# Performance work log

Measured on AMD Instinct MI355X. Metric: run time of the kernel, lower is better.

## Reference

```python
import jax, jax.numpy as jnp
import numpy as np

B, V, J, NB = 512, 6890, 24, 10
P = (J - 1) * 9  # 207 pose-blendshape features
# Standard SMPL kinematic tree (parents[0] = -1 for root)
PARENTS = np.array([-1, 0, 0, 0, 1, 2, 3, 4, 5, 6, 7, 8, 9, 9, 9, 12, 13, 14, 16, 17, 18, 19, 20, 21])


def rodrigues(aa):
    """Axis-angle [N,3] -> rotation matrices [N,3,3] (batch_rodrigues)."""
    angle = jnp.linalg.norm(aa, axis=-1, keepdims=True) + 1e-8
    axis = aa / angle
    x, y, z = axis[..., 0], axis[..., 1], axis[..., 2]
    zero = jnp.zeros_like(x)
    K = jnp.stack([zero, -z, y, z, zero, -x, -y, x, zero], axis=-1).reshape(aa.shape[0], 3, 3)
    s = jnp.sin(angle)[..., None]
    c = jnp.cos(angle)[..., None]
    return jnp.eye(3, dtype=aa.dtype) + s * K + (1.0 - c) * jnp.matmul(K, K)


def setup_inputs() -> dict:
    key = jax.random.key(0)
    ks = jax.random.split(key, 9)
    J_reg = jax.random.uniform(ks[7], (J, V), dtype=jnp.float32)
    J_reg = J_reg / jnp.sum(J_reg, axis=1, keepdims=True)
    W = jax.nn.softmax(4.0 * jax.random.normal(ks[8], (V, J), dtype=jnp.float32), axis=-1)
    return {
        "betas": jax.random.normal(ks[0], (B, NB), dtype=jnp.float32),
        "body_pose": 0.3 * jax.random.normal(ks[1], (B, (J - 1) * 3), dtype=jnp.float32),
        "global_orient": 0.3 * jax.random.normal(ks[2], (B, 3), dtype=jnp.float32),
        "transl": jax.random.normal(ks[3], (B, 3), dtype=jnp.float32),
        "v_template": jax.random.normal(ks[4], (V, 3), dtype=jnp.float32),
        "shapedirs": 0.01 * jax.random.normal(ks[5], (V, 3, NB), dtype=jnp.float32),
        "posedirs": 0.01 * jax.random.normal(ks[6], (P, V * 3), dtype=jnp.float32),
        "J_regressor": J_reg,
        "lbs_weights": W,
    }


def reference(betas, body_pose, global_orient, transl, v_template, shapedirs, posedirs, J_regressor, lbs_weights):
    b = betas.shape[0]
    # --- pose to rotation matrices (pose2rot=True path) ---
    full_pose = jnp.concatenate([global_orient, body_pose], axis=-1)  # [B, 72]
    rot_mats = rodrigues(full_pose.reshape(-1, 3)).reshape(b, J, 3, 3)
    # --- shape blend shapes ---
    v_shaped = v_template + jnp.einsum('bl,vcl->bvc', betas, shapedirs)  # [B,V,3]
    joints = jnp.einsum('jv,bvc->bjc', J_regressor, v_shaped)            # [B,J,3]
    # --- pose blend shapes ---
    pose_feature = (rot_mats[:, 1:] - jnp.eye(3, dtype=rot_mats.dtype)).reshape(b, P)
    v_posed = v_shaped + (pose_feature @ posedirs).reshape(b, V, 3)
    # --- kinematic chain (batch_rigid_transform) ---
    rel_joints = joints.at[:, 1:].add(-joints[:, PARENTS[1:]])
    top = jnp.concatenate([rot_mats, rel_joints[..., None]], axis=-1)   # [B,J,3,4]
    bottom = jnp.broadcast_to(jnp.array([0.0, 0.0, 0.0, 1.0], dtype=rot_mats.dtype), (b, J, 1, 4))
    mats = jnp.concatenate([top, bottom], axis=-2)                      # [B,J,4,4]
    chain = [mats[:, 0]]
    for i in range(1, J):  # fixed 24-joint serial composition
        chain.append(chain[PARENTS[i]] @ mats[:, i])
    A = jnp.stack(chain, axis=1)                                        # [B,J,4,4]
    posed_joints = A[..., :3, 3]
    # remove rest-pose joint locations from the transforms
    t_rel = A[..., :3, 3] - jnp.einsum('bjmn,bjn->bjm', A[..., :3, :3], joints)
    A_rel = A.at[..., :3, 3].set(t_rel)
    # --- linear blend skinning ---
    T = jnp.einsum('vj,bjmn->bvmn', lbs_weights, A_rel)                 # [B,V,4,4]
    verts = jnp.einsum('bvmn,bvn->bvm', T[..., :3, :3], v_posed) + T[..., :3, 3]
    vertices = verts + transl[:, None]
    joints_out = posed_joints + transl[:, None]
    return vertices, joints_out
```

## Files before the change

### kernel.cpp

```cpp
#include <hip/hip_runtime.h>
#include <hip/hip_bf16.h>
#include <math.h>

#define Bn 512
#define Vn 6890
#define NBn 10
#define Pn 207
#define N3n 20670
#define KP 224
#define VPAD 6912

typedef __attribute__((ext_vector_type(8))) _Float16 half8;
typedef __attribute__((ext_vector_type(4))) float f32x4;

__constant__ int c_par[24] = {-1,0,0,0,1,2,3,4,5,6,7,8,9,9,9,12,13,14,16,17,18,19,20,21};
__constant__ int c_lvl[10] = {0,1,4,7,10,15,18,20,22,24};


__global__ __launch_bounds__(256) void k_prep(
    const float* __restrict__ Jreg, const float* __restrict__ vtpl,
    const float* __restrict__ sdirs, const float* __restrict__ pdirs,
    const float* __restrict__ W, float* __restrict__ part,
    _Float16* __restrict__ B_h, _Float16* __restrict__ W_h)
{
  const int tid = threadIdx.x;
  if (blockIdx.x < 576) {
    const int bid = blockIdx.x % 72;
    const int chunk = blockIdx.x / 72;
    const int j = bid / 3, c = bid % 3;
    const int vlo = chunk * 862;
    const int vhi = min(Vn, vlo + 862);
    float acc[11];
#pragma unroll
    for (int k = 0; k < 11; k++) acc[k] = 0.f;
    for (int v = vlo + tid; v < vhi; v += 256) {
      float w = Jreg[(size_t)j * Vn + v];
      int n = v * 3 + c;
#pragma unroll
      for (int l = 0; l < 10; l++) acc[l] += w * sdirs[(size_t)n * 10 + l];
      acc[10] += w * vtpl[n];
    }
    __shared__ float red[256];
    for (int k = 0; k < 11; k++) {
      red[tid] = acc[k];
      __syncthreads();
      for (int s = 128; s > 0; s >>= 1) {
        if (tid < s) red[tid] += red[tid + s];
        __syncthreads();
      }
      if (tid == 0) part[(size_t)chunk * 792 + bid * 11 + k] = red[0];
      __syncthreads();
    }
  } else if (blockIdx.x < 576 + 2268) {
    const int pair = (blockIdx.x - 576) * 4 + (tid >> 6);
    const int l = tid & 63;
    const int nt = pair / 7, s = pair % 7;
    const int col = nt * 16 + (l & 15);
    const int kb = s * 32 + ((l >> 4) << 3);
    half8 hv;
#pragma unroll
    for (int j = 0; j < 8; j++) {
      int k = kb + j;
      float f = 0.f;
      if (col < N3n) {
        if (k < Pn) f = pdirs[(size_t)k * N3n + col];
        else if (k < 217) f = sdirs[(size_t)col * 10 + (k - 207)];
        else if (k == 217) f = (float)(_Float16)vtpl[col];
        else if (k == 218) {
          float t = vtpl[col];
          f = t - (float)(_Float16)t;
        }
      }
      hv[j] = (_Float16)f;
    }
    *(half8*)(B_h + (size_t)pair * 512 + l * 8) = hv;
  } else {
    int idx = (blockIdx.x - 576 - 2268) * 256 + tid;
    if (idx < VPAD * 32) {
      int v = idx >> 5, k = idx & 31;
      float f = (v < Vn && k < 24) ? W[(size_t)v * 24 + k] : 0.f;
      W_h[idx] = (_Float16)f;
    }
  }
}

__global__ __launch_bounds__(512) void k_pose2(
    const float* __restrict__ betas, const float* __restrict__ body_pose,
    const float* __restrict__ gorient, const float* __restrict__ transl,
    const float* __restrict__ part,
    _Float16* __restrict__ pf_h, _Float16* __restrict__ Ar_h,
    float* __restrict__ out_joints)
{
  const int tid = threadIdx.x;
  const int wave = tid >> 6;
  const int lane = tid & 63;
  const int b = blockIdx.x * 8 + wave;

  __shared__ float JS_s[720];
  __shared__ float Jt_s[72];
  __shared__ float Rs[8][24][9];
  __shared__ float jnt[8][24][3];
  __shared__ float rel[8][24][3];
  __shared__ float A_s[8][24][12];

  for (int idx = tid; idx < 792; idx += 512) {
    float s = 0.f;
#pragma unroll
    for (int y = 0; y < 8; y++) s += part[(size_t)y * 792 + idx];
    int bid = idx / 11, k = idx % 11;
    if (k < 10) JS_s[bid * 10 + k] = s;
    else        Jt_s[bid] = s;
  }

  if (lane < 24) {
    float x, y, z;
    if (lane == 0) { x = gorient[b*3+0]; y = gorient[b*3+1]; z = gorient[b*3+2]; }
    else { int o = b*69 + (lane-1)*3; x = body_pose[o]; y = body_pose[o+1]; z = body_pose[o+2]; }
    float ang = sqrtf(x*x + y*y + z*z) + 1e-8f;
    float inv = 1.0f / ang;
    float ux = x*inv, uy = y*inv, uz = z*inv;
    float s = sinf(ang), cc = cosf(ang), omc = 1.0f - cc;
    float K[9] = {0.f, -uz, uy,  uz, 0.f, -ux,  -uy, ux, 0.f};
#pragma unroll
    for (int mm = 0; mm < 3; mm++)
#pragma unroll
      for (int nn = 0; nn < 3; nn++) {
        float kk = K[mm*3+0]*K[0+nn] + K[mm*3+1]*K[3+nn] + K[mm*3+2]*K[6+nn];
        float eye = (mm == nn) ? 1.0f : 0.0f;
        Rs[wave][lane][mm*3+nn] = eye + s*K[mm*3+nn] + omc*kk;
      }
  }
  __syncthreads();

  for (int idx = lane; idx < 72; idx += 64) {
    float a = Jt_s[idx];
#pragma unroll
    for (int l = 0; l < 10; l++) a += betas[b*10 + l] * JS_s[idx*10 + l];
    jnt[wave][idx/3][idx%3] = a;
  }
  for (int idx = lane; idx < KP; idx += 64) {
    float f = 0.f;
    if (idx < Pn) {
      int j = 1 + idx / 9, e = idx % 9;
      float eye = (e == 0 || e == 4 || e == 8) ? 1.0f : 0.0f;
      f = Rs[wave][j][e] - eye;
    } else if (idx < 217) {
      f = betas[b*10 + (idx - 207)];
    } else if (idx < 219) {
      f = 1.0f;
    }
    pf_h[(size_t)b * KP + idx] = (_Float16)f;
  }
  __syncthreads();
  for (int idx = lane; idx < 72; idx += 64) {
    int j = idx/3, cc = idx%3;
    float r = jnt[wave][j][cc];
    if (j > 0) r -= jnt[wave][c_par[j]][cc];
    rel[wave][j][cc] = r;
  }
  __syncthreads();
  if (lane < 12) {
    int m = lane/4, nn = lane%4;
    A_s[wave][0][lane] = (nn < 3) ? Rs[wave][0][m*3+nn] : rel[wave][0][m];
  }
  __syncthreads();
  for (int lev = 1; lev <= 8; lev++) {
    const int s0 = c_lvl[lev], s1 = c_lvl[lev + 1];
    const int jj = lane / 12, r = lane % 12;
    if (jj < s1 - s0) {
      const int i = s0 + jj;
      const int p = c_par[i];
      const int m = r >> 2, nn = r & 3;
      float v;
      if (nn < 3)
        v = A_s[wave][p][m*4+0]*Rs[wave][i][0+nn] + A_s[wave][p][m*4+1]*Rs[wave][i][3+nn] + A_s[wave][p][m*4+2]*Rs[wave][i][6+nn];
      else
        v = A_s[wave][p][m*4+0]*rel[wave][i][0] + A_s[wave][p][m*4+1]*rel[wave][i][1] + A_s[wave][p][m*4+2]*rel[wave][i][2] + A_s[wave][p][m*4+3];
      A_s[wave][i][r] = v;
    }
    __syncthreads();
  }
  for (int idx = lane; idx < 72; idx += 64) {
    int j = idx/3, cc = idx%3;
    out_joints[(size_t)b * 72 + idx] = A_s[wave][j][cc*4+3] + transl[b*3+cc];
  }
  for (int idx = lane; idx < 512; idx += 64) {
    int e = idx >> 5, k = idx & 31;
    float a = 0.f;
    if (e < 12 && k < 24) {
      int m = e >> 2, nn = e & 3;
      if (nn < 3) a = A_s[wave][k][m*4+nn];
      else a = A_s[wave][k][m*4+3] - (A_s[wave][k][m*4+0]*jnt[wave][k][0] + A_s[wave][k][m*4+1]*jnt[wave][k][1] + A_s[wave][k][m*4+2]*jnt[wave][k][2]);
    }
    Ar_h[(size_t)b * 512 + idx] = (_Float16)a;
  }
}

__global__ __launch_bounds__(256) void k_mm3(
    const float* __restrict__ transl,
    const _Float16* __restrict__ pf_h, const _Float16* __restrict__ B_h,
    const _Float16* __restrict__ W_h, const _Float16* __restrict__ Ar_h,
    float* __restrict__ out)
{
  const int lin = blockIdx.x;
  const int r8 = lin & 7;
  const int k2 = lin >> 3;
  const int b_t = k2 & 7;
  const int m8 = k2 >> 3;
  const int v_t = r8 * 14 + m8;
  if (v_t >= 108) return;

  const int tid = threadIdx.x;
  const int l = tid & 63;
  const int wave = tid >> 6;
  const int b0 = b_t * 64;
  const int v0 = v_t * 64;

  __shared__ __align__(16) float vp[64][196];
  __shared__ float transl_s[64][3];

  if (tid < 192) transl_s[tid / 3][tid % 3] = transl[(size_t)b0 * 3 + tid];

  const int c0 = l & 15;
  const int kk0 = (l >> 4) << 3;
  const int ntb = v_t * 12 + wave * 3;
  f32x4 acc[4][3];
#pragma unroll
  for (int t = 0; t < 4; t++)
#pragma unroll
    for (int n = 0; n < 3; n++) acc[t][n] = (f32x4){0.f, 0.f, 0.f, 0.f};

#pragma unroll
  for (int s = 0; s < 7; s++) {
    half8 bv[3];
#pragma unroll
    for (int n = 0; n < 3; n++)
      bv[n] = *(const half8*)(B_h + ((size_t)(ntb + n) * 7 + s) * 512 + l * 8);
#pragma unroll
    for (int t = 0; t < 4; t++) {
      half8 fa = *(const half8*)(pf_h + (size_t)(b0 + t * 16 + c0) * KP + kk0 + s * 32);
#pragma unroll
      for (int n = 0; n < 3; n++)
        acc[t][n] = __builtin_amdgcn_mfma_f32_16x16x32_f16(fa, bv[n], acc[t][n], 0, 0, 0);
    }
  }
  {
    const int colb = wave * 48 + c0;
    const int rowb = (l >> 4) * 4;
#pragma unroll
    for (int t = 0; t < 4; t++)
#pragma unroll
      for (int n = 0; n < 3; n++)
#pragma unroll
        for (int r = 0; r < 4; r++)
          vp[t * 16 + rowb + r][colb + n * 16] = acc[t][n][r];
  }
  __syncthreads();

  const int c = l & 15;
  const int g = l >> 4;
  const int kk = g << 3;

  half8 wh[4];
#pragma unroll
  for (int mt = 0; mt < 4; mt++)
    wh[mt] = *(const half8*)(W_h + (size_t)(v0 + mt * 16 + c) * 32 + kk);

#pragma unroll
  for (int i = 0; i < 16; i++) {
    const int bl = wave * 16 + i;
    half8 ah = *(const half8*)(Ar_h + (size_t)(b0 + bl) * 512 + c * 32 + kk);
    const float trg = transl_s[bl][g < 3 ? g : 0];
#pragma unroll
    for (int mt = 0; mt < 4; mt++) {
      f32x4 t = {0.f, 0.f, 0.f, 0.f};
      t = __builtin_amdgcn_mfma_f32_16x16x32_f16(ah, wh[mt], t, 0, 0, 0);
      const int vl2 = mt * 16 + c;
      const int v = v0 + vl2;
      if (g < 3 && v < Vn) {
        float x = vp[bl][3 * vl2 + 0];
        float y = vp[bl][3 * vl2 + 1];
        float z = vp[bl][3 * vl2 + 2];
        out[((size_t)(b0 + bl) * Vn + v) * 3 + g] = t[0]*x + t[1]*y + t[2]*z + t[3] + trg;
      }
    }
  }
}


__global__ __launch_bounds__(256) void k_jsjt_part(
    const float* __restrict__ Jreg, const float* __restrict__ vtpl,
    const float* __restrict__ sdirs, float* __restrict__ part)
{
  const int bid = blockIdx.x;
  const int chunk = blockIdx.y;
  const int j = bid / 3, c = bid % 3;
  const int tid = threadIdx.x;
  const int vlo = chunk * 862;
  const int vhi = min(Vn, vlo + 862);
  float acc[11];
#pragma unroll
  for (int k = 0; k < 11; k++) acc[k] = 0.f;
  for (int v = vlo + tid; v < vhi; v += 256) {
    float w = Jreg[(size_t)j * Vn + v];
    int n = v * 3 + c;
#pragma unroll
    for (int l = 0; l < 10; l++) acc[l] += w * sdirs[(size_t)n * 10 + l];
    acc[10] += w * vtpl[n];
  }
  __shared__ float red[256];
  for (int k = 0; k < 11; k++) {
    red[tid] = acc[k];
    __syncthreads();
    for (int s = 128; s > 0; s >>= 1) {
      if (tid < s) red[tid] += red[tid + s];
      __syncthreads();
    }
    if (tid == 0) part[(size_t)chunk * 792 + bid * 11 + k] = red[0];
    __syncthreads();
  }
}

__global__ __launch_bounds__(1024) void k_jsjt_red(
    const float* __restrict__ part, float* __restrict__ JS, float* __restrict__ Jt)
{
  const int t = threadIdx.x;
  if (t >= 792) return;
  float s = 0.f;
#pragma unroll
  for (int y = 0; y < 8; y++) s += part[(size_t)y * 792 + t];
  int bid = t / 11, k = t % 11;
  if (k < 10) JS[bid * 10 + k] = s;
  else        Jt[bid] = s;
}

__global__ __launch_bounds__(64) void k_pose_fb(
    const float* __restrict__ betas, const float* __restrict__ body_pose,
    const float* __restrict__ gorient, const float* __restrict__ transl,
    const float* __restrict__ JS, const float* __restrict__ Jt,
    float* __restrict__ pf_ws, float* __restrict__ Ar_ws,
    float* __restrict__ out_joints)
{
  const int b = blockIdx.x;
  const int tid = threadIdx.x;
  __shared__ float Rs[24][9];
  __shared__ float jnt[24][3];
  __shared__ float rel[24][3];
  __shared__ float A_s[24][12];

  if (tid < 24) {
    float x, y, z;
    if (tid == 0) { x = gorient[b*3+0]; y = gorient[b*3+1]; z = gorient[b*3+2]; }
    else { int o = b*69 + (tid-1)*3; x = body_pose[o]; y = body_pose[o+1]; z = body_pose[o+2]; }
    float ang = sqrtf(x*x + y*y + z*z) + 1e-8f;
    float inv = 1.0f / ang;
    float ux = x*inv, uy = y*inv, uz = z*inv;
    float s = sinf(ang), cc = cosf(ang), omc = 1.0f - cc;
    float K[9] = {0.f, -uz, uy,  uz, 0.f, -ux,  -uy, ux, 0.f};
#pragma unroll
    for (int mm = 0; mm < 3; mm++)
#pragma unroll
      for (int nn = 0; nn < 3; nn++) {
        float kk = K[mm*3+0]*K[0+nn] + K[mm*3+1]*K[3+nn] + K[mm*3+2]*K[6+nn];
        float eye = (mm == nn) ? 1.0f : 0.0f;
        Rs[tid][mm*3+nn] = eye + s*K[mm*3+nn] + omc*kk;
      }
  }
  for (int idx = tid; idx < 72; idx += 64) {
    float a = Jt[idx];
#pragma unroll
    for (int l = 0; l < 10; l++) a += betas[b*10 + l] * JS[idx*10 + l];
    jnt[idx/3][idx%3] = a;
  }
  __syncthreads();
  for (int idx = tid; idx < Pn; idx += 64) {
    int j = 1 + idx / 9, e = idx % 9;
    float eye = (e == 0 || e == 4 || e == 8) ? 1.0f : 0.0f;
    pf_ws[(size_t)b * Pn + idx] = Rs[j][e] - eye;
  }
  for (int idx = tid; idx < 72; idx += 64) {
    int j = idx/3, cc = idx%3;
    float r = jnt[j][cc];
    if (j > 0) r -= jnt[c_par[j]][cc];
    rel[j][cc] = r;
  }
  __syncthreads();
  if (tid < 12) {
    int m = tid/4, nn = tid%4;
    A_s[0][tid] = (nn < 3) ? Rs[0][m*3+nn] : rel[0][m];
  }
  __syncthreads();
  for (int i = 1; i < 24; i++) {
    if (tid < 12) {
      int m = tid/4, nn = tid%4;
      int p = c_par[i];
      float v;
      if (nn < 3)
        v = A_s[p][m*4+0]*Rs[i][0+nn] + A_s[p][m*4+1]*Rs[i][3+nn] + A_s[p][m*4+2]*Rs[i][6+nn];
      else
        v = A_s[p][m*4+0]*rel[i][0] + A_s[p][m*4+1]*rel[i][1] + A_s[p][m*4+2]*rel[i][2] + A_s[p][m*4+3];
      A_s[i][tid] = v;
    }
    __syncthreads();
  }
  for (int idx = tid; idx < 72; idx += 64) {
    int j = idx/3, cc = idx%3;
    out_joints[(size_t)b * 72 + idx] = A_s[j][cc*4+3] + transl[b*3+cc];
  }
  for (int idx = tid; idx < 288; idx += 64) {
    int j = idx/12, r = idx%12, m = r/4, nn = r%4;
    float v;
    if (nn < 3) v = A_s[j][m*4+nn];
    else v = A_s[j][m*4+3] - (A_s[j][m*4+0]*jnt[j][0] + A_s[j][m*4+1]*jnt[j][1] + A_s[j][m*4+2]*jnt[j][2]);
    Ar_ws[(size_t)b * 288 + idx] = v;
  }
}

__global__ __launch_bounds__(192) void k_verts_fb(
    const float* __restrict__ betas, const float* __restrict__ transl,
    const float* __restrict__ vtpl, const float* __restrict__ sdirs,
    const float* __restrict__ pdirs, const float* __restrict__ W,
    const float* __restrict__ pf_ws, const float* __restrict__ Ar_ws,
    float* __restrict__ out)
{
  const int tid = threadIdx.x;
  const int b0 = blockIdx.x * 16;
  const int v0 = blockIdx.y * 128;
  const int n0 = v0 * 3;
  __shared__ __align__(16) float pf_s[Pn][16];
  __shared__ __align__(16) float Ar_s[16][288];
  __shared__ __align__(16) float vp_s[16][384];
  __shared__ float betas_s[16][NBn];
  __shared__ float transl_s[16][3];
  for (int idx = tid; idx < Pn * 16; idx += 192) {
    int p = idx >> 4, bi = idx & 15;
    pf_s[p][bi] = pf_ws[(size_t)(b0 + bi) * Pn + p];
  }
  for (int idx = tid; idx < 16 * 288; idx += 192)
    Ar_s[idx / 288][idx % 288] = Ar_ws[(size_t)b0 * 288 + idx];
  for (int idx = tid; idx < 16 * NBn; idx += 192)
    betas_s[idx / NBn][idx % NBn] = betas[(size_t)b0 * NBn + idx];
  for (int idx = tid; idx < 48; idx += 192)
    transl_s[idx / 3][idx % 3] = transl[(size_t)b0 * 3 + idx];
  __syncthreads();
  const int n = n0 + 2 * tid;
  const bool valid = (n < N3n);
  float acc0[16], acc1[16];
#pragma unroll
  for (int i = 0; i < 16; i++) { acc0[i] = 0.f; acc1[i] = 0.f; }
  for (int p = 0; p < Pn; p++) {
    float pd0 = 0.f, pd1 = 0.f;
    if (valid) { float2 t = *(const float2*)(pdirs + (size_t)p * N3n + n); pd0 = t.x; pd1 = t.y; }
    const float4* row = (const float4*)(pf_s[p]);
#pragma unroll
    for (int q = 0; q < 4; q++) {
      float4 f = row[q];
      acc0[4*q+0] += f.x * pd0;  acc1[4*q+0] += f.x * pd1;
      acc0[4*q+1] += f.y * pd0;  acc1[4*q+1] += f.y * pd1;
      acc0[4*q+2] += f.z * pd0;  acc1[4*q+2] += f.z * pd1;
      acc0[4*q+3] += f.w * pd0;  acc1[4*q+3] += f.w * pd1;
    }
  }
  float sd0[10], sd1[10], vt0 = 0.f, vt1 = 0.f;
#pragma unroll
  for (int l = 0; l < 10; l++) { sd0[l] = 0.f; sd1[l] = 0.f; }
  if (valid) {
    for (int l = 0; l < 10; l++) { sd0[l] = sdirs[(size_t)n*10 + l]; sd1[l] = sdirs[(size_t)n*10 + 10 + l]; }
    vt0 = vtpl[n]; vt1 = vtpl[n+1];
  }
#pragma unroll
  for (int bi = 0; bi < 16; bi++) {
    float s0 = vt0, s1 = vt1;
#pragma unroll
    for (int l = 0; l < 10; l++) { float bb = betas_s[bi][l]; s0 += bb*sd0[l]; s1 += bb*sd1[l]; }
    acc0[bi] += s0; acc1[bi] += s1;
  }
#pragma unroll
  for (int bi = 0; bi < 16; bi++) { vp_s[bi][2*tid] = acc0[bi]; vp_s[bi][2*tid+1] = acc1[bi]; }
  __syncthreads();
  const int m = tid / 64;
  const int vl = tid % 64;
  const int va = v0 + vl, vb = v0 + vl + 64;
  const bool va_ok = (va < Vn), vb_ok = (vb < Vn);
  float Wr0[24], Wr1[24];
#pragma unroll
  for (int j = 0; j < 24; j++) { Wr0[j] = 0.f; Wr1[j] = 0.f; }
  if (va_ok) { const float4* wp = (const float4*)(W + (size_t)va*24);
#pragma unroll
    for (int q = 0; q < 6; q++) { float4 f = wp[q]; Wr0[4*q]=f.x; Wr0[4*q+1]=f.y; Wr0[4*q+2]=f.z; Wr0[4*q+3]=f.w; } }
  if (vb_ok) { const float4* wp = (const float4*)(W + (size_t)vb*24);
#pragma unroll
    for (int q = 0; q < 6; q++) { float4 f = wp[q]; Wr1[4*q]=f.x; Wr1[4*q+1]=f.y; Wr1[4*q+2]=f.z; Wr1[4*q+3]=f.w; } }
  for (int bi = 0; bi < 16; bi++) {
    float Ta0=0.f,Ta1=0.f,Ta2=0.f,Ta3=0.f, Tb0=0.f,Tb1=0.f,Tb2=0.f,Tb3=0.f;
    const float4* arb = (const float4*)(Ar_s[bi]);
#pragma unroll
    for (int j = 0; j < 24; j++) {
      float4 a = arb[j*3 + m];
      float wa = Wr0[j], wb = Wr1[j];
      Ta0 += wa*a.x; Ta1 += wa*a.y; Ta2 += wa*a.z; Ta3 += wa*a.w;
      Tb0 += wb*a.x; Tb1 += wb*a.y; Tb2 += wb*a.z; Tb3 += wb*a.w;
    }
    float tr = transl_s[bi][m];
    if (va_ok) {
      float x = vp_s[bi][vl*3+0], y = vp_s[bi][vl*3+1], z = vp_s[bi][vl*3+2];
      out[((size_t)(b0+bi)*Vn + va)*3 + m] = Ta0*x + Ta1*y + Ta2*z + Ta3 + tr;
    }
    if (vb_ok) {
      float x = vp_s[bi][(vl+64)*3+0], y = vp_s[bi][(vl+64)*3+1], z = vp_s[bi][(vl+64)*3+2];
      out[((size_t)(b0+bi)*Vn + vb)*3 + m] = Tb0*x + Tb1*y + Tb2*z + Tb3 + tr;
    }
  }
}

extern "C" void kernel_launch(void* const* d_in, const int* in_sizes, int n_in,
                              void* d_out, int out_size, void* d_ws, size_t ws_size,
                              hipStream_t stream)
{
  const float *betas=nullptr, *bpose=nullptr, *gorient=nullptr, *transl=nullptr,
              *vtpl=nullptr, *sdirs=nullptr, *pdirs=nullptr, *Jreg=nullptr, *W=nullptr;
  int seen1536 = 0, seen165360 = 0;
  for (int i = 0; i < n_in; i++) {
    const float* p = (const float*)d_in[i];
    switch (in_sizes[i]) {
      case 5120:    betas = p; break;
      case 35328:   bpose = p; break;
      case 20670:   vtpl  = p; break;
      case 206700:  sdirs = p; break;
      case 4278690: pdirs = p; break;
      case 1536:    if (seen1536++ == 0) gorient = p; else transl = p; break;
      case 165360:  if (seen165360++ == 0) Jreg = p; else W = p; break;
      default: break;
    }
  }
  float* out = (float*)d_out;

  float* ws   = (float*)d_ws;
  float* part = ws;
  float* JS   = ws + 6336;
  float* Jt   = ws + 7056;
  float* pf   = ws + 7128;
  float* Ar   = ws + 113112;
  _Float16* pf_h = (_Float16*)(ws + 260568);
  _Float16* B_h  = (_Float16*)(ws + 317912);
  _Float16* W_h  = (_Float16*)(ws + 2640344);
  _Float16* Ar_h = (_Float16*)(ws + 2861528);
  const size_t WS_NEED = (size_t)3123672 * 4;
  const bool big = (ws_size >= WS_NEED);

  if (big) {
    k_prep<<<3708, 256, 0, stream>>>(Jreg, vtpl, sdirs, pdirs, W, part, B_h, W_h);
    k_pose2<<<64, 512, 0, stream>>>(betas, bpose, gorient, transl, part,
                                    pf_h, Ar_h, out + (size_t)Bn * Vn * 3);
    k_mm3<<<896, 256, 0, stream>>>(transl, pf_h, B_h, W_h, Ar_h, out);
  } else {
    k_jsjt_part<<<dim3(72, 8), 256, 0, stream>>>(Jreg, vtpl, sdirs, part);
    k_jsjt_red<<<1, 1024, 0, stream>>>(part, JS, Jt);
    k_pose_fb<<<Bn, 64, 0, stream>>>(betas, bpose, gorient, transl, JS, Jt, pf, Ar,
                                     out + (size_t)Bn * Vn * 3);
    k_verts_fb<<<dim3(32, 54), 192, 0, stream>>>(betas, transl, vtpl, sdirs,
                                                 pdirs, W, pf, Ar, out);
  }
}
```

Before: 59.89 us.

## Halve batch tile in fused skinning kernel, fp16 LDS staging, fold translation into weights

The main skinning kernel now processes 32 batch rows per block instead of 64 and launches twice as many blocks. It stores the posed-vertex staging buffer in LDS as fp16 instead of fp32, which cuts shared memory and should raise occupancy. The translation add is folded into the skinning MFMA through a constant-one weight column (k=24) paired with the translation in the transform matrix, so the separate per-block transl load goes away. The joint-regressor prep now handles all three coordinates per block using wave-shuffle reductions in place of a serial shared-memory tree, at the cost of more registers and some fp16 rounding of the posed vertices and translation.

```diff
diff --git a/kernel.cpp b/kernel.cpp
--- a/kernel.cpp
+++ b/kernel.cpp
@@ -24,35 +24,40 @@
     _Float16* __restrict__ B_h, _Float16* __restrict__ W_h)
 {
   const int tid = threadIdx.x;
-  if (blockIdx.x < 576) {
-    const int bid = blockIdx.x % 72;
-    const int chunk = blockIdx.x / 72;
-    const int j = bid / 3, c = bid % 3;
+  if (blockIdx.x < 192) {
+    const int j = blockIdx.x % 24;
+    const int chunk = blockIdx.x / 24;
+    const int lane = tid & 63, wv = tid >> 6;
     const int vlo = chunk * 862;
     const int vhi = min(Vn, vlo + 862);
-    float acc[11];
-#pragma unroll
-    for (int k = 0; k < 11; k++) acc[k] = 0.f;
+    __shared__ float wred[4][33];
+    float acc[33];
+#pragma unroll
+    for (int k = 0; k < 33; k++) acc[k] = 0.f;
     for (int v = vlo + tid; v < vhi; v += 256) {
       float w = Jreg[(size_t)j * Vn + v];
-      int n = v * 3 + c;
-#pragma unroll
-      for (int l = 0; l < 10; l++) acc[l] += w * sdirs[(size_t)n * 10 + l];
-      acc[10] += w * vtpl[n];
-    }
-    __shared__ float red[256];
-    for (int k = 0; k < 11; k++) {
-      red[tid] = acc[k];
-      __syncthreads();
-      for (int s = 128; s > 0; s >>= 1) {
-        if (tid < s) red[tid] += red[tid + s];
-        __syncthreads();
+      const float* sp = sdirs + (size_t)v * 30;
+#pragma unroll
+      for (int c = 0; c < 3; c++) {
+#pragma unroll
+        for (int l = 0; l < 10; l++) acc[c*11 + l] += w * sp[c*10 + l];
+        acc[c*11 + 10] += w * vtpl[v*3 + c];
       }
-      if (tid == 0) part[(size_t)chunk * 792 + bid * 11 + k] = red[0];
-      __syncthreads();
-    }
-  } else if (blockIdx.x < 576 + 2268) {
-    const int pair = (blockIdx.x - 576) * 4 + (tid >> 6);
+    }
+#pragma unroll
+    for (int k = 0; k < 33; k++) {
+      float s = acc[k];
+      for (int off = 32; off > 0; off >>= 1) s += __shfl_xor(s, off);
+      if (lane == 0) wred[wv][k] = s;
+    }
+    __syncthreads();
+    if (tid < 33) {
+      float s = wred[0][tid] + wred[1][tid] + wred[2][tid] + wred[3][tid];
+      int c = tid / 11, k = tid % 11;
+      part[(size_t)chunk * 792 + (j*3 + c) * 11 + k] = s;
+    }
+  } else if (blockIdx.x < 192 + 2268) {
+    const int pair = (blockIdx.x - 192) * 4 + (tid >> 6);
     const int l = tid & 63;
     const int nt = pair / 7, s = pair % 7;
     const int col = nt * 16 + (l & 15);
@@ -75,10 +80,13 @@
     }
     *(half8*)(B_h + (size_t)pair * 512 + l * 8) = hv;
   } else {
-    int idx = (blockIdx.x - 576 - 2268) * 256 + tid;
+    int idx = (blockIdx.x - 192 - 2268) * 256 + tid;
     if (idx < VPAD * 32) {
       int v = idx >> 5, k = idx & 31;
-      float f = (v < Vn && k < 24) ? W[(size_t)v * 24 + k] : 0.f;
+      float f;
+      if (v < Vn && k < 24) f = W[(size_t)v * 24 + k];
+      else if (k == 24)     f = 1.0f;
+      else                  f = 0.f;
       W_h[idx] = (_Float16)f;
     }
   }
@@ -191,13 +199,14 @@
       int m = e >> 2, nn = e & 3;
       if (nn < 3) a = A_s[wave][k][m*4+nn];
       else a = A_s[wave][k][m*4+3] - (A_s[wave][k][m*4+0]*jnt[wave][k][0] + A_s[wave][k][m*4+1]*jnt[wave][k][1] + A_s[wave][k][m*4+2]*jnt[wave][k][2]);
+    } else if (k == 24 && e < 12 && (e & 3) == 3) {
+      a = transl[b*3 + (e >> 2)];
     }
     Ar_h[(size_t)b * 512 + idx] = (_Float16)a;
   }
 }
 
-__global__ __launch_bounds__(256) void k_mm3(
-    const float* __restrict__ transl,
+__global__ __launch_bounds__(256) void k_mm4(
     const _Float16* __restrict__ pf_h, const _Float16* __restrict__ B_h,
     const _Float16* __restrict__ W_h, const _Float16* __restrict__ Ar_h,
     float* __restrict__ out)
@@ -205,28 +214,25 @@
   const int lin = blockIdx.x;
   const int r8 = lin & 7;
   const int k2 = lin >> 3;
-  const int b_t = k2 & 7;
-  const int m8 = k2 >> 3;
+  const int b_t = k2 & 15;
+  const int m8 = k2 >> 4;
   const int v_t = r8 * 14 + m8;
   if (v_t >= 108) return;
 
   const int tid = threadIdx.x;
   const int l = tid & 63;
   const int wave = tid >> 6;
-  const int b0 = b_t * 64;
+  const int b0 = b_t * 32;
   const int v0 = v_t * 64;
 
-  __shared__ __align__(16) float vp[64][196];
-  __shared__ float transl_s[64][3];
-
-  if (tid < 192) transl_s[tid / 3][tid % 3] = transl[(size_t)b0 * 3 + tid];
+  __shared__ __align__(16) _Float16 vp[32][196];
 
   const int c0 = l & 15;
   const int kk0 = (l >> 4) << 3;
   const int ntb = v_t * 12 + wave * 3;
-  f32x4 acc[4][3];
-#pragma unroll
-  for (int t = 0; t < 4; t++)
+  f32x4 acc[2][3];
+#pragma unroll
+  for (int t = 0; t < 2; t++)
 #pragma unroll
     for (int n = 0; n < 3; n++) acc[t][n] = (f32x4){0.f, 0.f, 0.f, 0.f};
 
@@ -237,7 +243,7 @@
     for (int n = 0; n < 3; n++)
       bv[n] = *(const half8*)(B_h + ((size_t)(ntb + n) * 7 + s) * 512 + l * 8);
 #pragma unroll
-    for (int t = 0; t < 4; t++) {
+    for (int t = 0; t < 2; t++) {
       half8 fa = *(const half8*)(pf_h + (size_t)(b0 + t * 16 + c0) * KP + kk0 + s * 32);
 #pragma unroll
       for (int n = 0; n < 3; n++)
@@ -248,12 +254,12 @@
     const int colb = wave * 48 + c0;
     const int rowb = (l >> 4) * 4;
 #pragma unroll
-    for (int t = 0; t < 4; t++)
+    for (int t = 0; t < 2; t++)
 #pragma unroll
       for (int n = 0; n < 3; n++)
 #pragma unroll
         for (int r = 0; r < 4; r++)
-          vp[t * 16 + rowb + r][colb + n * 16] = acc[t][n][r];
+          vp[t * 16 + rowb + r][colb + n * 16] = (_Float16)acc[t][n][r];
   }
   __syncthreads();
 
@@ -267,10 +273,9 @@
     wh[mt] = *(const half8*)(W_h + (size_t)(v0 + mt * 16 + c) * 32 + kk);
 
 #pragma unroll
-  for (int i = 0; i < 16; i++) {
-    const int bl = wave * 16 + i;
+  for (int i = 0; i < 8; i++) {
+    const int bl = wave * 8 + i;
     half8 ah = *(const half8*)(Ar_h + (size_t)(b0 + bl) * 512 + c * 32 + kk);
-    const float trg = transl_s[bl][g < 3 ? g : 0];
 #pragma unroll
     for (int mt = 0; mt < 4; mt++) {
       f32x4 t = {0.f, 0.f, 0.f, 0.f};
@@ -278,10 +283,10 @@
       const int vl2 = mt * 16 + c;
       const int v = v0 + vl2;
       if (g < 3 && v < Vn) {
-        float x = vp[bl][3 * vl2 + 0];
-        float y = vp[bl][3 * vl2 + 1];
-        float z = vp[bl][3 * vl2 + 2];
-        out[((size_t)(b0 + bl) * Vn + v) * 3 + g] = t[0]*x + t[1]*y + t[2]*z + t[3] + trg;
+        float x = (float)vp[bl][3 * vl2 + 0];
+        float y = (float)vp[bl][3 * vl2 + 1];
+        float z = (float)vp[bl][3 * vl2 + 2];
+        out[((size_t)(b0 + bl) * Vn + v) * 3 + g] = t[0]*x + t[1]*y + t[2]*z + t[3];
       }
     }
   }
@@ -549,10 +554,10 @@
   const bool big = (ws_size >= WS_NEED);
 
   if (big) {
-    k_prep<<<3708, 256, 0, stream>>>(Jreg, vtpl, sdirs, pdirs, W, part, B_h, W_h);
+    k_prep<<<3324, 256, 0, stream>>>(Jreg, vtpl, sdirs, pdirs, W, part, B_h, W_h);
     k_pose2<<<64, 512, 0, stream>>>(betas, bpose, gorient, transl, part,
                                     pf_h, Ar_h, out + (size_t)Bn * Vn * 3);
-    k_mm3<<<896, 256, 0, stream>>>(transl, pf_h, B_h, W_h, Ar_h, out);
+    k_mm4<<<1792, 256, 0, stream>>>(pf_h, B_h, W_h, Ar_h, out);
   } else {
     k_jsjt_part<<<dim3(72, 8), 256, 0, stream>>>(Jreg, vtpl, sdirs, part);
     k_jsjt_red<<<1, 1024, 0, stream>>>(part, JS, Jt);
```

Result: faster. 58.64 us (-2.1%).
